# Kernel optimization log

Measured on AMD Instinct MI355X. Metric: run time of the kernel, lower is better.

The kernel has to match this reference:

```python
import jax, jax.numpy as jnp
import numpy as np

N = 50000        # nodes
E = 800000       # edges (avg degree 16)
F_IN = 128       # in_channels
HID = 32         # hidden_channels per head
H = 8            # heads
DH = HID * H     # 256, concat dim
NC = {'TL': 12, 'YL': 30, 'TS': 60, 'TZ': 120}
NEG_SLOPE = 0.2  # PyG GATConv default


def setup_inputs() -> dict:
    key = jax.random.key(0)
    ks = jax.random.split(key, 40)
    rn = lambda k, s, sc=0.1: jax.random.normal(k, s, jnp.float32) * sc
    inp = {}
    inp['x'] = jax.random.normal(ks[0], (N, F_IN), jnp.float32)
    inp['edge_index'] = jax.random.randint(ks[1], (2, E), 0, N, dtype=jnp.int64)
    # conv1: in -> H x HID (concat)
    inp['W1'] = rn(ks[2], (F_IN, DH)); inp['a1s'] = rn(ks[3], (H, HID)); inp['a1d'] = rn(ks[4], (H, HID)); inp['b1'] = jnp.zeros((DH,), jnp.float32)
    # conv2: DH -> H x HID (concat)
    inp['W2'] = rn(ks[5], (DH, DH)); inp['a2s'] = rn(ks[6], (H, HID)); inp['a2d'] = rn(ks[7], (H, HID)); inp['b2'] = jnp.zeros((DH,), jnp.float32)
    # task heads: DH -> C, heads=1, concat=False
    i = 8
    for t, c in NC.items():
        inp['W_' + t] = rn(ks[i], (DH, c)); i += 1
        inp['as_' + t] = rn(ks[i], (1, c)); i += 1
        inp['ad_' + t] = rn(ks[i], (1, c)); i += 1
        inp['b_' + t] = jnp.zeros((c,), jnp.float32)
    return inp


def gat_conv(x, src, dst, W, a_s, a_d, b, concat):
    """PyG-style GATConv (eval mode, self-loops already in src/dst)."""
    n = x.shape[0]
    heads, out_ch = a_s.shape
    h = (x @ W).reshape(n, heads, out_ch)                 # [N,H,C]
    alpha_s = jnp.einsum('nhc,hc->nh', h, a_s)            # [N,H]
    alpha_d = jnp.einsum('nhc,hc->nh', h, a_d)
    e = jax.nn.leaky_relu(alpha_s[src] + alpha_d[dst], NEG_SLOPE)   # [E,H]
    # numerically-stable segment softmax over incoming edges of each dst
    m = jax.ops.segment_max(e, dst, num_segments=n)
    ex = jnp.exp(e - m[dst])
    denom = jax.ops.segment_sum(ex, dst, num_segments=n)
    alpha = ex / (denom[dst] + 1e-16)                     # [E,H]
    out = jax.ops.segment_sum(alpha[:, :, None] * h[src], dst, num_segments=n)  # [N,H,C]
    out = out.reshape(n, heads * out_ch) if concat else out.mean(axis=1)
    return out + b


def reference(x, edge_index, W1, a1s, a1d, b1, W2, a2s, a2d, b2,
              W_TL, as_TL, ad_TL, b_TL, W_YL, as_YL, ad_YL, b_YL,
              W_TS, as_TS, ad_TS, b_TS, W_TZ, as_TZ, ad_TZ, b_TZ):
    n = x.shape[0]
    loop = jnp.arange(n, dtype=edge_index.dtype)
    src = jnp.concatenate([edge_index[0], loop])
    dst = jnp.concatenate([edge_index[1], loop])
    h = jax.nn.elu(gat_conv(x, src, dst, W1, a1s, a1d, b1, True))
    h = gat_conv(h, src, dst, W2, a2s, a2d, b2, True)
    tl = jax.nn.log_softmax(gat_conv(h, src, dst, W_TL, as_TL, ad_TL, b_TL, False), axis=1)
    yl = jax.nn.log_softmax(gat_conv(h, src, dst, W_YL, as_YL, ad_YL, b_YL, False), axis=1)
    ts = jax.nn.log_softmax(gat_conv(h, src, dst, W_TS, as_TS, ad_TS, b_TS, False), axis=1)
    tz = jax.nn.log_softmax(gat_conv(h, src, dst, W_TZ, as_TZ, ad_TZ, b_TZ, False), axis=1)
    return (tl, yl, ts, tz)
```

## Files before the change

### kernel.cpp

```cpp
#include <hip/hip_runtime.h>
#include <math.h>


#define NEG_SLOPE 0.2f

typedef short s8v __attribute__((ext_vector_type(8)));
typedef short s4v __attribute__((ext_vector_type(4)));
typedef float f4v __attribute__((ext_vector_type(4)));

__device__ __forceinline__ short f2bf(float x) {
    unsigned u = __float_as_uint(x);
    u += 0x7fffu + ((u >> 16) & 1u);
    return (short)(u >> 16);
}
__device__ __forceinline__ float bf2f(short b) {
    return __uint_as_float(((unsigned)(unsigned short)b) << 16);
}
__device__ __forceinline__ void split2(float x, short& h, short& l) {
    h = f2bf(x);
    l = f2bf(x - bf2f(h));
}
__device__ __forceinline__ float4 bf4_to_f4(s4v v) {
    return make_float4(bf2f(v[0]), bf2f(v[1]), bf2f(v[2]), bf2f(v[3]));
}


__global__ void init_kernel(int* __restrict__ deg, int* __restrict__ cursor, int n) {
    int i = blockIdx.x * blockDim.x + threadIdx.x;
    if (i < n) { deg[i] = 1; cursor[i] = 0; }
}

__global__ void count_kernel(const int* __restrict__ dst, int* __restrict__ deg, int E) {
    int i = blockIdx.x * blockDim.x + threadIdx.x;
    if (i < E) atomicAdd(&deg[dst[i]], 1);
}

__global__ __launch_bounds__(1024) void scan_kernel(const int* __restrict__ deg,
                                                    int* __restrict__ rowstart, int n) {
    __shared__ int sh[1024];
    __shared__ int carry_sh;
    if (threadIdx.x == 0) { carry_sh = 0; rowstart[0] = 0; }
    __syncthreads();
    for (int base = 0; base < n; base += 8192) {
        int vals[8];
        int sum = 0;
        int i0 = base + threadIdx.x * 8;
        #pragma unroll
        for (int j = 0; j < 8; ++j) {
            int i = i0 + j;
            int v = (i < n) ? deg[i] : 0;
            sum += v;
            vals[j] = sum;
        }
        sh[threadIdx.x] = sum;
        __syncthreads();
        for (int off = 1; off < 1024; off <<= 1) {
            int t = (threadIdx.x >= (unsigned)off) ? sh[threadIdx.x - off] : 0;
            __syncthreads();
            sh[threadIdx.x] += t;
            __syncthreads();
        }
        int excl = sh[threadIdx.x] - sum + carry_sh;
        #pragma unroll
        for (int j = 0; j < 8; ++j) {
            int i = i0 + j;
            if (i < n) rowstart[i + 1] = excl + vals[j];
        }
        __syncthreads();
        if (threadIdx.x == 0) carry_sh += sh[1023];
        __syncthreads();
    }
}

__global__ void scatter_kernel(const int* __restrict__ src, const int* __restrict__ dst,
                               const int* __restrict__ rowstart, int* __restrict__ cursor,
                               int* __restrict__ csr, int* __restrict__ csrd, int E, int n) {
    int i = blockIdx.x * blockDim.x + threadIdx.x;
    if (i >= E + n) return;
    int s, d;
    if (i < E) { s = src[i]; d = dst[i]; }
    else       { s = d = i - E; }
    int p = atomicAdd(&cursor[d], 1);
    int slot = rowstart[d] + p;
    csr[slot] = s;
    csrd[slot] = d;
}


__global__ void split_a_kernel(const float* __restrict__ A, short* __restrict__ Ah,
                               short* __restrict__ Al, int n4) {
    int i = blockIdx.x * blockDim.x + threadIdx.x;
    if (i >= n4) return;
    float4 v = ((const float4*)A)[i];
    short h0, h1, h2, h3, l0, l1, l2, l3;
    split2(v.x, h0, l0); split2(v.y, h1, l1);
    split2(v.z, h2, l2); split2(v.w, h3, l3);
    s4v hv = {h0, h1, h2, h3};
    s4v lv = {l0, l1, l2, l3};
    ((s4v*)Ah)[i] = hv;
    ((s4v*)Al)[i] = lv;
}

__global__ void split_bt_kernel(const float* __restrict__ B, short* __restrict__ Bh,
                                short* __restrict__ Bl, int K, int Nc, int kshift) {
    int idx = blockIdx.x * blockDim.x + threadIdx.x;
    if (idx >= Nc * K) return;
    int n = idx >> kshift;
    int k = idx & (K - 1);
    float v = B[(size_t)k * Nc + n];
    short h, l; split2(v, h, l);
    Bh[idx] = h;
    Bl[idx] = l;
}

__global__ void fold_alpha8_kernel(const float* __restrict__ W,
                                   const float* __restrict__ a_s, const float* __restrict__ a_d,
                                   short* __restrict__ Bth, short* __restrict__ Btl,
                                   int K, int Nfeat) {
    int idx = blockIdx.x * blockDim.x + threadIdx.x;
    if (idx >= K * 16) return;
    int j = idx / K, k = idx % K;
    int h = j & 7;
    const float* av = ((j < 8) ? a_s : a_d) + h * 32;
    const float* wp = W + (size_t)k * 256 + h * 32;
    float s = 0.f;
    #pragma unroll
    for (int c = 0; c < 32; ++c) s += wp[c] * av[c];
    short hi, lo; split2(s, hi, lo);
    size_t off = (size_t)(Nfeat + j) * K + k;
    Bth[off] = hi; Btl[off] = lo;
}

__global__ void fold_alpha4_kernel(const float* __restrict__ Wcat,
                                   const float* __restrict__ ascat, const float* __restrict__ adcat,
                                   short* __restrict__ Bth, short* __restrict__ Btl) {
    int idx = blockIdx.x * blockDim.x + threadIdx.x;
    if (idx >= 256 * 8) return;
    int j = idx >> 8, k = idx & 255;
    const int CO[4] = {0, 12, 42, 102};
    const int CL[4] = {12, 30, 60, 120};
    int t = j & 3;
    const float* av = ((j < 4) ? ascat : adcat) + CO[t];
    const float* wp = Wcat + (size_t)k * 222 + CO[t];
    float s = 0.f;
    for (int c = 0; c < CL[t]; ++c) s += wp[c] * av[c];
    short hi, lo; split2(s, hi, lo);
    size_t off = (size_t)(222 + j) * 256 + k;
    Bth[off] = hi; Btl[off] = lo;
}


#define MB 128
#define NB 64
#define KS 32

__global__ __launch_bounds__(256) void gemm_mfma_kernel(
        const short* __restrict__ Ah_g, const short* __restrict__ Al_g,
        const short* __restrict__ Bth_g, const short* __restrict__ Btl_g,
        short* __restrict__ Cb, int cb_stride,
        float* __restrict__ als, float* __restrict__ ald, int nsplit,
        int M, int K, int Nfeat, int NcExt) {
    __shared__ __align__(16) short Ah[MB][40];
    __shared__ __align__(16) short Al[MB][40];
    __shared__ __align__(16) short Bh[NB][40];
    __shared__ __align__(16) short Bl[NB][40];

    int t = threadIdx.x;
    int lane = t & 63, w = t >> 6;
    int quad = lane >> 4, l16 = lane & 15;
    int row0 = blockIdx.y * MB, col0 = blockIdx.x * NB;

    f4v acc[2][4];
    #pragma unroll
    for (int mt = 0; mt < 2; ++mt)
        #pragma unroll
        for (int nt = 0; nt < 4; ++nt)
            acc[mt][nt] = (f4v){0.f, 0.f, 0.f, 0.f};

    for (int k0 = 0; k0 < K; k0 += KS) {
        __syncthreads();
        #pragma unroll
        for (int i = 0; i < 2; ++i) {
            int u = i * 256 + t;
            int r = u >> 2, kk = (u & 3) * 8;
            int gr = row0 + r;
            s8v vh = {0, 0, 0, 0, 0, 0, 0, 0};
            s8v vl = {0, 0, 0, 0, 0, 0, 0, 0};
            if (gr < M) {
                vh = *(const s8v*)(Ah_g + (size_t)gr * K + k0 + kk);
                vl = *(const s8v*)(Al_g + (size_t)gr * K + k0 + kk);
            }
            *(s8v*)&Ah[r][kk] = vh;
            *(s8v*)&Al[r][kk] = vl;
        }
        {
            int n = t >> 2, kk = (t & 3) * 8;
            int gc = col0 + n;
            s8v vh = {0, 0, 0, 0, 0, 0, 0, 0};
            s8v vl = {0, 0, 0, 0, 0, 0, 0, 0};
            if (gc < NcExt) {
                vh = *(const s8v*)(Bth_g + (size_t)gc * K + k0 + kk);
                vl = *(const s8v*)(Btl_g + (size_t)gc * K + k0 + kk);
            }
            *(s8v*)&Bh[n][kk] = vh;
            *(s8v*)&Bl[n][kk] = vl;
        }
        __syncthreads();

        int kb = quad * 8;
        s8v a_h[2], a_l[2], b_h[4], b_l[4];
        #pragma unroll
        for (int mt = 0; mt < 2; ++mt) {
            int r = w * 32 + mt * 16 + l16;
            a_h[mt] = *(const s8v*)&Ah[r][kb];
            a_l[mt] = *(const s8v*)&Al[r][kb];
        }
        #pragma unroll
        for (int nt = 0; nt < 4; ++nt) {
            int c = nt * 16 + l16;
            b_h[nt] = *(const s8v*)&Bh[c][kb];
            b_l[nt] = *(const s8v*)&Bl[c][kb];
        }
        #pragma unroll
        for (int mt = 0; mt < 2; ++mt)
            #pragma unroll
            for (int nt = 0; nt < 4; ++nt) {
                acc[mt][nt] = __builtin_amdgcn_mfma_f32_16x16x32_bf16(
                    a_h[mt], b_h[nt], acc[mt][nt], 0, 0, 0);
                acc[mt][nt] = __builtin_amdgcn_mfma_f32_16x16x32_bf16(
                    a_h[mt], b_l[nt], acc[mt][nt], 0, 0, 0);
                acc[mt][nt] = __builtin_amdgcn_mfma_f32_16x16x32_bf16(
                    a_l[mt], b_h[nt], acc[mt][nt], 0, 0, 0);
            }
    }

    #pragma unroll
    for (int mt = 0; mt < 2; ++mt) {
        #pragma unroll
        for (int nt = 0; nt < 4; ++nt) {
            int gc = col0 + nt * 16 + l16;
            if (gc >= NcExt) continue;
            #pragma unroll
            for (int r = 0; r < 4; ++r) {
                int gr = row0 + w * 32 + mt * 16 + quad * 4 + r;
                if (gr >= M) continue;
                float v = acc[mt][nt][r];
                if (gc < Nfeat) {
                    Cb[(size_t)gr * cb_stride + gc] = f2bf(v);
                } else {
                    int j = gc - Nfeat;
                    if (j < nsplit)            als[(size_t)gr * nsplit + j] = v;
                    else if (j < 2 * nsplit)   ald[(size_t)gr * nsplit + (j - nsplit)] = v;
                }
            }
        }
    }
}


__global__ void ew8_kernel(const float* __restrict__ als, const float* __restrict__ ald,
                           const int* __restrict__ csr, const int* __restrict__ csrd,
                           float* __restrict__ ew, int M) {
    int i = blockIdx.x * blockDim.x + threadIdx.x;
    if (i >= M) return;
    int s = csr[i], d = csrd[i];
    const float4* ap = (const float4*)(als + (size_t)s * 8);
    const float4* dp = (const float4*)(ald + (size_t)d * 8);
    float4 a0 = ap[0], a1 = ap[1];
    float4 d0 = dp[0], d1 = dp[1];
    float v[8] = {a0.x + d0.x, a0.y + d0.y, a0.z + d0.z, a0.w + d0.w,
                  a1.x + d1.x, a1.y + d1.y, a1.z + d1.z, a1.w + d1.w};
    float w[8];
    #pragma unroll
    for (int h = 0; h < 8; ++h) {
        float x = v[h];
        x = (x > 0.f) ? x : NEG_SLOPE * x;
        w[h] = __expf(x);
    }
    float4* op = (float4*)(ew + (size_t)i * 8);
    op[0] = make_float4(w[0], w[1], w[2], w[3]);
    op[1] = make_float4(w[4], w[5], w[6], w[7]);
}


__global__ __launch_bounds__(256) void gat_gather_kernel(
        const short* __restrict__ hb, const float* __restrict__ ew,
        const int* __restrict__ rowstart, const int* __restrict__ csr,
        const float* __restrict__ bias, short* __restrict__ oh, short* __restrict__ ol,
        int n, int elu) {
    int wid  = blockIdx.x * 4 + (threadIdx.x >> 6);
    int lane = threadIdx.x & 63;
    if (wid >= n) return;
    int row = rowstart[wid];
    int deg = rowstart[wid + 1] - row;
    int hp = lane >> 3;
    int ch = lane * 4;
    const int* cp = csr + row;
    const float* wp = ew + (size_t)row * 8 + hp;

    float4 acc = {0.f, 0.f, 0.f, 0.f};
    float wsum = 0.f;
    int e = 0;
    for (; e + 4 <= deg; e += 4) {
        int s0 = cp[e], s1 = cp[e + 1], s2 = cp[e + 2], s3 = cp[e + 3];
        float w0 = wp[(size_t)(e + 0) * 8];
        float w1 = wp[(size_t)(e + 1) * 8];
        float w2 = wp[(size_t)(e + 2) * 8];
        float w3 = wp[(size_t)(e + 3) * 8];
        float4 h0 = bf4_to_f4(*(const s4v*)(hb + (size_t)s0 * 256 + ch));
        float4 h1 = bf4_to_f4(*(const s4v*)(hb + (size_t)s1 * 256 + ch));
        float4 h2 = bf4_to_f4(*(const s4v*)(hb + (size_t)s2 * 256 + ch));
        float4 h3 = bf4_to_f4(*(const s4v*)(hb + (size_t)s3 * 256 + ch));
        acc.x += w0 * h0.x + w1 * h1.x + w2 * h2.x + w3 * h3.x;
        acc.y += w0 * h0.y + w1 * h1.y + w2 * h2.y + w3 * h3.y;
        acc.z += w0 * h0.z + w1 * h1.z + w2 * h2.z + w3 * h3.z;
        acc.w += w0 * h0.w + w1 * h1.w + w2 * h2.w + w3 * h3.w;
        wsum += (w0 + w1) + (w2 + w3);
    }
    for (; e < deg; ++e) {
        int s0 = cp[e];
        float w0 = wp[(size_t)e * 8];
        float4 h0 = bf4_to_f4(*(const s4v*)(hb + (size_t)s0 * 256 + ch));
        acc.x += w0 * h0.x; acc.y += w0 * h0.y;
        acc.z += w0 * h0.z; acc.w += w0 * h0.w;
        wsum += w0;
    }
    float inv = 1.f / (wsum + 1e-16f);
    float4 b4 = *(const float4*)(bias + ch);
    float v[4] = {acc.x * inv + b4.x, acc.y * inv + b4.y,
                  acc.z * inv + b4.z, acc.w * inv + b4.w};
    if (elu) {
        #pragma unroll
        for (int j = 0; j < 4; ++j)
            v[j] = (v[j] > 0.f) ? v[j] : __expf(v[j]) - 1.f;
    }
    s4v hv, lv;
    #pragma unroll
    for (int j = 0; j < 4; ++j) { short hh, ll; split2(v[j], hh, ll); hv[j] = hh; lv[j] = ll; }
    *(s4v*)(oh + (size_t)wid * 256 + ch) = hv;
    *(s4v*)(ol + (size_t)wid * 256 + ch) = lv;
}


__global__ void pack_w_kernel(const float* __restrict__ wTL, const float* __restrict__ wYL,
                              const float* __restrict__ wTS, const float* __restrict__ wTZ,
                              const float* __restrict__ bTL, const float* __restrict__ bYL,
                              const float* __restrict__ bTS, const float* __restrict__ bTZ,
                              const float* __restrict__ asTL, const float* __restrict__ asYL,
                              const float* __restrict__ asTS, const float* __restrict__ asTZ,
                              const float* __restrict__ adTL, const float* __restrict__ adYL,
                              const float* __restrict__ adTS, const float* __restrict__ adTZ,
                              float* __restrict__ Wcat, float* __restrict__ bcat,
                              float* __restrict__ ascat, float* __restrict__ adcat) {
    int idx = blockIdx.x * blockDim.x + threadIdx.x;
    if (idx < 256 * 222) {
        int r = idx / 222, c = idx % 222;
        float v;
        if (c < 12)       v = wTL[r * 12 + c];
        else if (c < 42)  v = wYL[r * 30 + (c - 12)];
        else if (c < 102) v = wTS[r * 60 + (c - 42)];
        else              v = wTZ[r * 120 + (c - 102)];
        Wcat[idx] = v;
    }
    if (idx < 222) {
        bcat[idx]  = (idx < 12) ? bTL[idx] : (idx < 42) ? bYL[idx - 12]
                   : (idx < 102) ? bTS[idx - 42] : bTZ[idx - 102];
        ascat[idx] = (idx < 12) ? asTL[idx] : (idx < 42) ? asYL[idx - 12]
                   : (idx < 102) ? asTS[idx - 42] : asTZ[idx - 102];
        adcat[idx] = (idx < 12) ? adTL[idx] : (idx < 42) ? adYL[idx - 12]
                   : (idx < 102) ? adTS[idx - 42] : adTZ[idx - 102];
    }
}


__global__ void ew4_kernel(const float* __restrict__ ast, const float* __restrict__ adt,
                           const int* __restrict__ csr, const int* __restrict__ csrd,
                           float* __restrict__ ew, int M) {
    int i = blockIdx.x * blockDim.x + threadIdx.x;
    if (i >= M) return;
    int s = csr[i], d = csrd[i];
    float4 a = *(const float4*)(ast + (size_t)s * 4);
    float4 b = *(const float4*)(adt + (size_t)d * 4);
    float v[4] = {a.x + b.x, a.y + b.y, a.z + b.z, a.w + b.w};
    float w[4];
    #pragma unroll
    for (int t = 0; t < 4; ++t) {
        float x = v[t];
        x = (x > 0.f) ? x : NEG_SLOPE * x;
        w[t] = __expf(x);
    }
    *(float4*)(ew + (size_t)i * 4) = make_float4(w[0], w[1], w[2], w[3]);
}


__global__ __launch_bounds__(256) void task_gather_ls_kernel(
        const short* __restrict__ htb, const float* __restrict__ ew,
        const int* __restrict__ rowstart, const int* __restrict__ csr,
        const float* __restrict__ bcat, float* __restrict__ out, int n) {
    int wid  = blockIdx.x * 4 + (threadIdx.x >> 6);
    int lane = threadIdx.x & 63;
    if (wid >= n) return;
    int row = rowstart[wid];
    int deg = rowstart[wid + 1] - row;
    int ch0 = lane * 4;
    const int CO[4] = {0, 12, 42, 102};
    const int CL[4] = {12, 30, 60, 120};

    int tj[4]; bool valj[4];
    #pragma unroll
    for (int j = 0; j < 4; ++j) {
        int ch = ch0 + j;
        valj[j] = (ch < 222);
        tj[j] = (ch >= 102) ? 3 : (ch >= 42) ? 2 : (ch >= 12) ? 1 : 0;
    }
    int t_lo = tj[0], t_hi = tj[3];
    bool use_lo[4];
    #pragma unroll
    for (int j = 0; j < 4; ++j) use_lo[j] = (tj[j] == t_lo);

    const int* cp = csr + row;
    const float* wp = ew + (size_t)row * 4;

    float acc[4] = {0.f, 0.f, 0.f, 0.f};
    float ws_lo = 0.f, ws_hi = 0.f;
    int e = 0;
    for (; e + 4 <= deg; e += 4) {
        int s0 = cp[e], s1 = cp[e + 1], s2 = cp[e + 2], s3 = cp[e + 3];
        float wlo0 = wp[(size_t)(e + 0) * 4 + t_lo], whi0 = wp[(size_t)(e + 0) * 4 + t_hi];
        float wlo1 = wp[(size_t)(e + 1) * 4 + t_lo], whi1 = wp[(size_t)(e + 1) * 4 + t_hi];
        float wlo2 = wp[(size_t)(e + 2) * 4 + t_lo], whi2 = wp[(size_t)(e + 2) * 4 + t_hi];
        float wlo3 = wp[(size_t)(e + 3) * 4 + t_lo], whi3 = wp[(size_t)(e + 3) * 4 + t_hi];
        float4 h0 = bf4_to_f4(*(const s4v*)(htb + (size_t)s0 * 224 + ch0));
        float4 h1 = bf4_to_f4(*(const s4v*)(htb + (size_t)s1 * 224 + ch0));
        float4 h2 = bf4_to_f4(*(const s4v*)(htb + (size_t)s2 * 224 + ch0));
        float4 h3 = bf4_to_f4(*(const s4v*)(htb + (size_t)s3 * 224 + ch0));
        ws_lo += (wlo0 + wlo1) + (wlo2 + wlo3);
        ws_hi += (whi0 + whi1) + (whi2 + whi3);
        float hv0[4] = {h0.x, h0.y, h0.z, h0.w};
        float hv1[4] = {h1.x, h1.y, h1.z, h1.w};
        float hv2[4] = {h2.x, h2.y, h2.z, h2.w};
        float hv3[4] = {h3.x, h3.y, h3.z, h3.w};
        #pragma unroll
        for (int j = 0; j < 4; ++j) {
            float w0 = use_lo[j] ? wlo0 : whi0;
            float w1 = use_lo[j] ? wlo1 : whi1;
            float w2 = use_lo[j] ? wlo2 : whi2;
            float w3 = use_lo[j] ? wlo3 : whi3;
            acc[j] += w0 * hv0[j] + w1 * hv1[j] + w2 * hv2[j] + w3 * hv3[j];
        }
    }
    for (; e < deg; ++e) {
        int s = cp[e];
        float wlo = wp[(size_t)e * 4 + t_lo];
        float whi = wp[(size_t)e * 4 + t_hi];
        ws_lo += wlo; ws_hi += whi;
        float4 h0 = bf4_to_f4(*(const s4v*)(htb + (size_t)s * 224 + ch0));
        float hv[4] = {h0.x, h0.y, h0.z, h0.w};
        #pragma unroll
        for (int j = 0; j < 4; ++j) {
            float w = use_lo[j] ? wlo : whi;
            acc[j] += w * hv[j];
        }
    }
    float inv_lo = 1.f / (ws_lo + 1e-16f);
    float inv_hi = 1.f / (ws_hi + 1e-16f);

    float vout[4];
    float m4[4] = {-1e30f, -1e30f, -1e30f, -1e30f};
    #pragma unroll
    for (int j = 0; j < 4; ++j) {
        if (valj[j]) {
            float v = acc[j] * (use_lo[j] ? inv_lo : inv_hi) + bcat[ch0 + j];
            vout[j] = v;
            m4[tj[j]] = fmaxf(m4[tj[j]], v);
        } else vout[j] = 0.f;
    }
    #pragma unroll
    for (int off = 1; off < 64; off <<= 1)
        #pragma unroll
        for (int t = 0; t < 4; ++t) m4[t] = fmaxf(m4[t], __shfl_xor(m4[t], off));
    float s4a[4] = {0.f, 0.f, 0.f, 0.f};
    #pragma unroll
    for (int j = 0; j < 4; ++j)
        if (valj[j]) s4a[tj[j]] += __expf(vout[j] - m4[tj[j]]);
    #pragma unroll
    for (int off = 1; off < 64; off <<= 1)
        #pragma unroll
        for (int t = 0; t < 4; ++t) s4a[t] += __shfl_xor(s4a[t], off);
    float lse[4];
    #pragma unroll
    for (int t = 0; t < 4; ++t) lse[t] = m4[t] + __logf(s4a[t]);
    #pragma unroll
    for (int j = 0; j < 4; ++j) {
        if (!valj[j]) continue;
        int t = tj[j];
        out[(size_t)CO[t] * n + (size_t)wid * CL[t] + (ch0 + j - CO[t])] = vout[j] - lse[t];
    }
}


extern "C" void kernel_launch(void* const* d_in, const int* in_sizes, int n_in,
                              void* d_out, int out_size, void* d_ws, size_t ws_size,
                              hipStream_t stream) {
    const float* x   = (const float*)d_in[0];
    const int*   ei  = (const int*)d_in[1];
    const float* W1  = (const float*)d_in[2];
    const float* a1s = (const float*)d_in[3];
    const float* a1d = (const float*)d_in[4];
    const float* b1  = (const float*)d_in[5];
    const float* W2  = (const float*)d_in[6];
    const float* a2s = (const float*)d_in[7];
    const float* a2d = (const float*)d_in[8];
    const float* b2  = (const float*)d_in[9];
    const float* W_TL = (const float*)d_in[10]; const float* as_TL = (const float*)d_in[11];
    const float* ad_TL = (const float*)d_in[12]; const float* b_TL = (const float*)d_in[13];
    const float* W_YL = (const float*)d_in[14]; const float* as_YL = (const float*)d_in[15];
    const float* ad_YL = (const float*)d_in[16]; const float* b_YL = (const float*)d_in[17];
    const float* W_TS = (const float*)d_in[18]; const float* as_TS = (const float*)d_in[19];
    const float* ad_TS = (const float*)d_in[20]; const float* b_TS = (const float*)d_in[21];
    const float* W_TZ = (const float*)d_in[22]; const float* as_TZ = (const float*)d_in[23];
    const float* ad_TZ = (const float*)d_in[24]; const float* b_TZ = (const float*)d_in[25];

    const int N = in_sizes[0] / 128;
    const int E = in_sizes[1] / 2;
    const int* e_src = ei;
    const int* e_dst = ei + E;
    const int M = E + N;

    float* ws = (float*)d_ws;
    float* B1   = ws;
    float* B2   = B1 + (size_t)N * 256;
    float* B3   = B2 + (size_t)N * 256;
    float* as1  = B3 + (size_t)N * 256;
    float* ad1  = as1 + (size_t)N * 8;
    float* as2  = ad1 + (size_t)N * 8;
    float* ad2  = as2 + (size_t)N * 8;
    float* ast  = ad2 + (size_t)N * 8;
    float* adt  = ast + (size_t)N * 4;
    float* Wcat = adt + (size_t)N * 4;
    float* bcat = Wcat + 256 * 222;
    float* ascat = bcat + 224;
    float* adcat = ascat + 224;
    int* deg      = (int*)(adcat + 224);
    int* rowstart = deg + N;
    int* cursor   = rowstart + (N + 1);
    int* csr      = cursor + N;
    int* csrd     = csr + M;
    uintptr_t wsp = (uintptr_t)(csrd + M);
    wsp = (wsp + 15) & ~(uintptr_t)15;
    short* W1h = (short*)wsp;
    short* W1l = W1h + 272 * 128;
    short* W2h = W1l + 272 * 128;
    short* W2l = W2h + 272 * 256;
    short* Wth = W2l + 272 * 256;
    short* Wtl = Wth + 230 * 256;
    short* Xh  = (short*)B1;
    short* Xl  = Xh + (size_t)N * 128;
    short* Sh  = (short*)B1;
    short* Sl  = Sh + (size_t)N * 256;
    short* Th  = (short*)B1;
    short* Tl  = Th + (size_t)N * 256;
    short* h1b = (short*)B2;
    short* h2b = (short*)B2;
    short* htb = (short*)B2;
    float* ew1 = B3;
    float* ew2 = B3;
    float* ewt = B3;

    float* out = (float*)d_out;

    const int B = 256;
    init_kernel<<<(N + B - 1) / B, B, 0, stream>>>(deg, cursor, N);
    count_kernel<<<(E + B - 1) / B, B, 0, stream>>>(e_dst, deg, E);
    scan_kernel<<<1, 1024, 0, stream>>>(deg, rowstart, N);
    scatter_kernel<<<(M + B - 1) / B, B, 0, stream>>>(e_src, e_dst, rowstart, cursor, csr, csrd, E, N);
    pack_w_kernel<<<(256 * 222 + B - 1) / B, B, 0, stream>>>(W_TL, W_YL, W_TS, W_TZ,
        b_TL, b_YL, b_TS, b_TZ, as_TL, as_YL, as_TS, as_TZ, ad_TL, ad_YL, ad_TS, ad_TZ,
        Wcat, bcat, ascat, adcat);
    split_bt_kernel<<<(256 * 128 + B - 1) / B, B, 0, stream>>>(W1, W1h, W1l, 128, 256, 7);
    split_bt_kernel<<<(256 * 256 + B - 1) / B, B, 0, stream>>>(W2, W2h, W2l, 256, 256, 8);
    split_bt_kernel<<<(222 * 256 + B - 1) / B, B, 0, stream>>>(Wcat, Wth, Wtl, 256, 222, 8);
    fold_alpha8_kernel<<<(128 * 16 + B - 1) / B, B, 0, stream>>>(W1, a1s, a1d, W1h, W1l, 128, 256);
    fold_alpha8_kernel<<<(256 * 16 + B - 1) / B, B, 0, stream>>>(W2, a2s, a2d, W2h, W2l, 256, 256);
    fold_alpha4_kernel<<<(256 * 8 + B - 1) / B, B, 0, stream>>>(Wcat, ascat, adcat, Wth, Wtl);
    split_a_kernel<<<((N * 128 / 4) + B - 1) / B, B, 0, stream>>>(x, Xh, Xl, N * 128 / 4);
    {
        dim3 g((272 + NB - 1) / NB, (N + MB - 1) / MB);
        gemm_mfma_kernel<<<g, 256, 0, stream>>>(Xh, Xl, W1h, W1l, h1b, 256,
                                                as1, ad1, 8, N, 128, 256, 272);
    }
    ew8_kernel<<<(M + B - 1) / B, B, 0, stream>>>(as1, ad1, csr, csrd, ew1, M);
    gat_gather_kernel<<<(N + 3) / 4, 256, 0, stream>>>(h1b, ew1, rowstart, csr, b1, Sh, Sl, N, 1);
    {
        dim3 g((272 + NB - 1) / NB, (N + MB - 1) / MB);
        gemm_mfma_kernel<<<g, 256, 0, stream>>>(Sh, Sl, W2h, W2l, h2b, 256,
                                                as2, ad2, 8, N, 256, 256, 272);
    }
    ew8_kernel<<<(M + B - 1) / B, B, 0, stream>>>(as2, ad2, csr, csrd, ew2, M);
    gat_gather_kernel<<<(N + 3) / 4, 256, 0, stream>>>(h2b, ew2, rowstart, csr, b2, Th, Tl, N, 0);
    {
        dim3 g((230 + NB - 1) / NB, (N + MB - 1) / MB);
        gemm_mfma_kernel<<<g, 256, 0, stream>>>(Th, Tl, Wth, Wtl, htb, 224,
                                                ast, adt, 4, N, 256, 222, 230);
    }
    ew4_kernel<<<(M + B - 1) / B, B, 0, stream>>>(ast, adt, csr, csrd, ewt, M);
    task_gather_ls_kernel<<<(N + 3) / 4, 256, 0, stream>>>(htb, ewt, rowstart, csr, bcat, out, N);
}
```

Before: 710.4 us.

## Drop low-part bf16 split of activations and simplify task log-softmax reductions

Activations fed to the three GEMMs are now rounded to a single bf16 value, not split into hi/lo parts. This removes the lo arrays, their global writes and reads, the lo LDS tile, and one of the three MFMAs per tile. Weights keep their hi/lo split. Separately, the task-head log-softmax drops its dynamically indexed per-task arrays in favour of lo/hi selects, to avoid private-memory spills. Accuracy falls to roughly bf16 on the activation side, which risks tolerance failures.

```diff
diff --git a/kernel.cpp b/kernel.cpp
--- a/kernel.cpp
+++ b/kernel.cpp
@@ -87,18 +87,12 @@
 }
 
 
-__global__ void split_a_kernel(const float* __restrict__ A, short* __restrict__ Ah,
-                               short* __restrict__ Al, int n4) {
+__global__ void tobf_kernel(const float* __restrict__ A, short* __restrict__ Ah, int n4) {
     int i = blockIdx.x * blockDim.x + threadIdx.x;
     if (i >= n4) return;
     float4 v = ((const float4*)A)[i];
-    short h0, h1, h2, h3, l0, l1, l2, l3;
-    split2(v.x, h0, l0); split2(v.y, h1, l1);
-    split2(v.z, h2, l2); split2(v.w, h3, l3);
-    s4v hv = {h0, h1, h2, h3};
-    s4v lv = {l0, l1, l2, l3};
+    s4v hv = {f2bf(v.x), f2bf(v.y), f2bf(v.z), f2bf(v.w)};
     ((s4v*)Ah)[i] = hv;
-    ((s4v*)Al)[i] = lv;
 }
 
 __global__ void split_bt_kernel(const float* __restrict__ B, short* __restrict__ Bh,
@@ -155,13 +149,12 @@
 #define KS 32
 
 __global__ __launch_bounds__(256) void gemm_mfma_kernel(
-        const short* __restrict__ Ah_g, const short* __restrict__ Al_g,
+        const short* __restrict__ Ah_g,
         const short* __restrict__ Bth_g, const short* __restrict__ Btl_g,
         short* __restrict__ Cb, int cb_stride,
         float* __restrict__ als, float* __restrict__ ald, int nsplit,
         int M, int K, int Nfeat, int NcExt) {
     __shared__ __align__(16) short Ah[MB][40];
-    __shared__ __align__(16) short Al[MB][40];
     __shared__ __align__(16) short Bh[NB][40];
     __shared__ __align__(16) short Bl[NB][40];
 
@@ -185,13 +178,8 @@
             int r = u >> 2, kk = (u & 3) * 8;
             int gr = row0 + r;
             s8v vh = {0, 0, 0, 0, 0, 0, 0, 0};
-            s8v vl = {0, 0, 0, 0, 0, 0, 0, 0};
-            if (gr < M) {
-                vh = *(const s8v*)(Ah_g + (size_t)gr * K + k0 + kk);
-                vl = *(const s8v*)(Al_g + (size_t)gr * K + k0 + kk);
-            }
+            if (gr < M) vh = *(const s8v*)(Ah_g + (size_t)gr * K + k0 + kk);
             *(s8v*)&Ah[r][kk] = vh;
-            *(s8v*)&Al[r][kk] = vl;
         }
         {
             int n = t >> 2, kk = (t & 3) * 8;
@@ -208,12 +196,11 @@
         __syncthreads();
 
         int kb = quad * 8;
-        s8v a_h[2], a_l[2], b_h[4], b_l[4];
+        s8v a_f[2], b_h[4], b_l[4];
         #pragma unroll
         for (int mt = 0; mt < 2; ++mt) {
             int r = w * 32 + mt * 16 + l16;
-            a_h[mt] = *(const s8v*)&Ah[r][kb];
-            a_l[mt] = *(const s8v*)&Al[r][kb];
+            a_f[mt] = *(const s8v*)&Ah[r][kb];
         }
         #pragma unroll
         for (int nt = 0; nt < 4; ++nt) {
@@ -226,11 +213,9 @@
             #pragma unroll
             for (int nt = 0; nt < 4; ++nt) {
                 acc[mt][nt] = __builtin_amdgcn_mfma_f32_16x16x32_bf16(
-                    a_h[mt], b_h[nt], acc[mt][nt], 0, 0, 0);
+                    a_f[mt], b_h[nt], acc[mt][nt], 0, 0, 0);
                 acc[mt][nt] = __builtin_amdgcn_mfma_f32_16x16x32_bf16(
-                    a_h[mt], b_l[nt], acc[mt][nt], 0, 0, 0);
-                acc[mt][nt] = __builtin_amdgcn_mfma_f32_16x16x32_bf16(
-                    a_l[mt], b_h[nt], acc[mt][nt], 0, 0, 0);
+                    a_f[mt], b_l[nt], acc[mt][nt], 0, 0, 0);
             }
     }
 
@@ -286,8 +271,7 @@
 __global__ __launch_bounds__(256) void gat_gather_kernel(
         const short* __restrict__ hb, const float* __restrict__ ew,
         const int* __restrict__ rowstart, const int* __restrict__ csr,
-        const float* __restrict__ bias, short* __restrict__ oh, short* __restrict__ ol,
-        int n, int elu) {
+        const float* __restrict__ bias, short* __restrict__ oh, int n, int elu) {
     int wid  = blockIdx.x * 4 + (threadIdx.x >> 6);
     int lane = threadIdx.x & 63;
     if (wid >= n) return;
@@ -334,11 +318,8 @@
         for (int j = 0; j < 4; ++j)
             v[j] = (v[j] > 0.f) ? v[j] : __expf(v[j]) - 1.f;
     }
-    s4v hv, lv;
-    #pragma unroll
-    for (int j = 0; j < 4; ++j) { short hh, ll; split2(v[j], hh, ll); hv[j] = hh; lv[j] = ll; }
+    s4v hv = {f2bf(v[0]), f2bf(v[1]), f2bf(v[2]), f2bf(v[3])};
     *(s4v*)(oh + (size_t)wid * 256 + ch) = hv;
-    *(s4v*)(ol + (size_t)wid * 256 + ch) = lv;
 }
 
 
@@ -393,6 +374,13 @@
 }
 
 
+__device__ __forceinline__ float sel4(int t, float v0, float v1, float v2, float v3) {
+    return (t == 0) ? v0 : (t == 1) ? v1 : (t == 2) ? v2 : v3;
+}
+__device__ __forceinline__ int sel4i(int t, int v0, int v1, int v2, int v3) {
+    return (t == 0) ? v0 : (t == 1) ? v1 : (t == 2) ? v2 : v3;
+}
+
 __global__ __launch_bounds__(256) void task_gather_ls_kernel(
         const short* __restrict__ htb, const float* __restrict__ ew,
         const int* __restrict__ rowstart, const int* __restrict__ csr,
@@ -403,20 +391,22 @@
     int row = rowstart[wid];
     int deg = rowstart[wid + 1] - row;
     int ch0 = lane * 4;
-    const int CO[4] = {0, 12, 42, 102};
-    const int CL[4] = {12, 30, 60, 120};
-
-    int tj[4]; bool valj[4];
-    #pragma unroll
-    for (int j = 0; j < 4; ++j) {
-        int ch = ch0 + j;
-        valj[j] = (ch < 222);
-        tj[j] = (ch >= 102) ? 3 : (ch >= 42) ? 2 : (ch >= 12) ? 1 : 0;
-    }
-    int t_lo = tj[0], t_hi = tj[3];
-    bool use_lo[4];
-    #pragma unroll
-    for (int j = 0; j < 4; ++j) use_lo[j] = (tj[j] == t_lo);
+
+    bool valj[4]; bool lo_j[4];
+    int t_lo, t_hi;
+    {
+        int tj0 = (ch0 >= 102) ? 3 : (ch0 >= 42) ? 2 : (ch0 >= 12) ? 1 : 0;
+        int ch3 = ch0 + 3;
+        int tj3 = (ch3 >= 102) ? 3 : (ch3 >= 42) ? 2 : (ch3 >= 12) ? 1 : 0;
+        t_lo = tj0; t_hi = tj3;
+        #pragma unroll
+        for (int j = 0; j < 4; ++j) {
+            int ch = ch0 + j;
+            valj[j] = (ch < 222);
+            int tj = (ch >= 102) ? 3 : (ch >= 42) ? 2 : (ch >= 12) ? 1 : 0;
+            lo_j[j] = (tj == t_lo);
+        }
+    }
 
     const int* cp = csr + row;
     const float* wp = ew + (size_t)row * 4;
@@ -442,10 +432,10 @@
         float hv3[4] = {h3.x, h3.y, h3.z, h3.w};
         #pragma unroll
         for (int j = 0; j < 4; ++j) {
-            float w0 = use_lo[j] ? wlo0 : whi0;
-            float w1 = use_lo[j] ? wlo1 : whi1;
-            float w2 = use_lo[j] ? wlo2 : whi2;
-            float w3 = use_lo[j] ? wlo3 : whi3;
+            float w0 = lo_j[j] ? wlo0 : whi0;
+            float w1 = lo_j[j] ? wlo1 : whi1;
+            float w2 = lo_j[j] ? wlo2 : whi2;
+            float w3 = lo_j[j] ? wlo3 : whi3;
             acc[j] += w0 * hv0[j] + w1 * hv1[j] + w2 * hv2[j] + w3 * hv3[j];
         }
     }
@@ -457,44 +447,69 @@
         float4 h0 = bf4_to_f4(*(const s4v*)(htb + (size_t)s * 224 + ch0));
         float hv[4] = {h0.x, h0.y, h0.z, h0.w};
         #pragma unroll
-        for (int j = 0; j < 4; ++j) {
-            float w = use_lo[j] ? wlo : whi;
-            acc[j] += w * hv[j];
-        }
+        for (int j = 0; j < 4; ++j)
+            acc[j] += (lo_j[j] ? wlo : whi) * hv[j];
     }
     float inv_lo = 1.f / (ws_lo + 1e-16f);
     float inv_hi = 1.f / (ws_hi + 1e-16f);
 
     float vout[4];
-    float m4[4] = {-1e30f, -1e30f, -1e30f, -1e30f};
+    float m_lo = -1e30f, m_hi = -1e30f;
+    #pragma unroll
+    for (int j = 0; j < 4; ++j) {
+        float v = 0.f;
+        if (valj[j]) {
+            v = acc[j] * (lo_j[j] ? inv_lo : inv_hi) + bcat[ch0 + j];
+            if (lo_j[j]) m_lo = fmaxf(m_lo, v); else m_hi = fmaxf(m_hi, v);
+        }
+        vout[j] = v;
+    }
+    float m0 = -1e30f, m1 = -1e30f, m2 = -1e30f, m3 = -1e30f;
+    m0 = (t_lo == 0) ? fmaxf(m0, m_lo) : m0;  m0 = (t_hi == 0) ? fmaxf(m0, m_hi) : m0;
+    m1 = (t_lo == 1) ? fmaxf(m1, m_lo) : m1;  m1 = (t_hi == 1) ? fmaxf(m1, m_hi) : m1;
+    m2 = (t_lo == 2) ? fmaxf(m2, m_lo) : m2;  m2 = (t_hi == 2) ? fmaxf(m2, m_hi) : m2;
+    m3 = (t_lo == 3) ? fmaxf(m3, m_lo) : m3;  m3 = (t_hi == 3) ? fmaxf(m3, m_hi) : m3;
+    #pragma unroll
+    for (int off = 1; off < 64; off <<= 1) {
+        m0 = fmaxf(m0, __shfl_xor(m0, off));
+        m1 = fmaxf(m1, __shfl_xor(m1, off));
+        m2 = fmaxf(m2, __shfl_xor(m2, off));
+        m3 = fmaxf(m3, __shfl_xor(m3, off));
+    }
+    float mt_lo = sel4(t_lo, m0, m1, m2, m3);
+    float mt_hi = sel4(t_hi, m0, m1, m2, m3);
+    float s_lo = 0.f, s_hi = 0.f;
     #pragma unroll
     for (int j = 0; j < 4; ++j) {
         if (valj[j]) {
-            float v = acc[j] * (use_lo[j] ? inv_lo : inv_hi) + bcat[ch0 + j];
-            vout[j] = v;
-            m4[tj[j]] = fmaxf(m4[tj[j]], v);
-        } else vout[j] = 0.f;
-    }
-    #pragma unroll
-    for (int off = 1; off < 64; off <<= 1)
-        #pragma unroll
-        for (int t = 0; t < 4; ++t) m4[t] = fmaxf(m4[t], __shfl_xor(m4[t], off));
-    float s4a[4] = {0.f, 0.f, 0.f, 0.f};
-    #pragma unroll
-    for (int j = 0; j < 4; ++j)
-        if (valj[j]) s4a[tj[j]] += __expf(vout[j] - m4[tj[j]]);
-    #pragma unroll
-    for (int off = 1; off < 64; off <<= 1)
-        #pragma unroll
-        for (int t = 0; t < 4; ++t) s4a[t] += __shfl_xor(s4a[t], off);
-    float lse[4];
-    #pragma unroll
-    for (int t = 0; t < 4; ++t) lse[t] = m4[t] + __logf(s4a[t]);
+            if (lo_j[j]) s_lo += __expf(vout[j] - mt_lo);
+            else         s_hi += __expf(vout[j] - mt_hi);
+        }
+    }
+    float s0 = ((t_lo == 0) ? s_lo : 0.f) + ((t_hi == 0 && t_hi != t_lo) ? s_hi : 0.f);
+    float s1 = ((t_lo == 1) ? s_lo : 0.f) + ((t_hi == 1 && t_hi != t_lo) ? s_hi : 0.f);
+    float s2 = ((t_lo == 2) ? s_lo : 0.f) + ((t_hi == 2 && t_hi != t_lo) ? s_hi : 0.f);
+    float s3 = ((t_lo == 3) ? s_lo : 0.f) + ((t_hi == 3 && t_hi != t_lo) ? s_hi : 0.f);
+    #pragma unroll
+    for (int off = 1; off < 64; off <<= 1) {
+        s0 += __shfl_xor(s0, off);
+        s1 += __shfl_xor(s1, off);
+        s2 += __shfl_xor(s2, off);
+        s3 += __shfl_xor(s3, off);
+    }
+    float l0 = m0 + __logf(s0), l1 = m1 + __logf(s1);
+    float l2 = m2 + __logf(s2), l3 = m3 + __logf(s3);
+    float lse_lo = sel4(t_lo, l0, l1, l2, l3);
+    float lse_hi = sel4(t_hi, l0, l1, l2, l3);
+    int co_lo = sel4i(t_lo, 0, 12, 42, 102), cl_lo = sel4i(t_lo, 12, 30, 60, 120);
+    int co_hi = sel4i(t_hi, 0, 12, 42, 102), cl_hi = sel4i(t_hi, 12, 30, 60, 120);
     #pragma unroll
     for (int j = 0; j < 4; ++j) {
         if (!valj[j]) continue;
-        int t = tj[j];
-        out[(size_t)CO[t] * n + (size_t)wid * CL[t] + (ch0 + j - CO[t])] = vout[j] - lse[t];
+        int co = lo_j[j] ? co_lo : co_hi;
+        int cl = lo_j[j] ? cl_lo : cl_hi;
+        float lse = lo_j[j] ? lse_lo : lse_hi;
+        out[(size_t)co * n + (size_t)wid * cl + (ch0 + j - co)] = vout[j] - lse;
     }
 }
 
@@ -555,11 +570,8 @@
     short* Wth = W2l + 272 * 256;
     short* Wtl = Wth + 230 * 256;
     short* Xh  = (short*)B1;
-    short* Xl  = Xh + (size_t)N * 128;
     short* Sh  = (short*)B1;
-    short* Sl  = Sh + (size_t)N * 256;
     short* Th  = (short*)B1;
-    short* Tl  = Th + (size_t)N * 256;
     short* h1b = (short*)B2;
     short* h2b = (short*)B2;
     short* htb = (short*)B2;
@@ -583,24 +595,24 @@
     fold_alpha8_kernel<<<(128 * 16 + B - 1) / B, B, 0, stream>>>(W1, a1s, a1d, W1h, W1l, 128, 256);
     fold_alpha8_kernel<<<(256 * 16 + B - 1) / B, B, 0, stream>>>(W2, a2s, a2d, W2h, W2l, 256, 256);
     fold_alpha4_kernel<<<(256 * 8 + B - 1) / B, B, 0, stream>>>(Wcat, ascat, adcat, Wth, Wtl);
-    split_a_kernel<<<((N * 128 / 4) + B - 1) / B, B, 0, stream>>>(x, Xh, Xl, N * 128 / 4);
+    tobf_kernel<<<((N * 128 / 4) + B - 1) / B, B, 0, stream>>>(x, Xh, N * 128 / 4);
     {
         dim3 g((272 + NB - 1) / NB, (N + MB - 1) / MB);
-        gemm_mfma_kernel<<<g, 256, 0, stream>>>(Xh, Xl, W1h, W1l, h1b, 256,
+        gemm_mfma_kernel<<<g, 256, 0, stream>>>(Xh, W1h, W1l, h1b, 256,
                                                 as1, ad1, 8, N, 128, 256, 272);
     }
     ew8_kernel<<<(M + B - 1) / B, B, 0, stream>>>(as1, ad1, csr, csrd, ew1, M);
-    gat_gather_kernel<<<(N + 3) / 4, 256, 0, stream>>>(h1b, ew1, rowstart, csr, b1, Sh, Sl, N, 1);
+    gat_gather_kernel<<<(N + 3) / 4, 256, 0, stream>>>(h1b, ew1, rowstart, csr, b1, Sh, N, 1);
     {
         dim3 g((272 + NB - 1) / NB, (N + MB - 1) / MB);
-        gemm_mfma_kernel<<<g, 256, 0, stream>>>(Sh, Sl, W2h, W2l, h2b, 256,
+        gemm_mfma_kernel<<<g, 256, 0, stream>>>(Sh, W2h, W2l, h2b, 256,
                                                 as2, ad2, 8, N, 256, 256, 272);
     }
     ew8_kernel<<<(M + B - 1) / B, B, 0, stream>>>(as2, ad2, csr, csrd, ew2, M);
-    gat_gather_kernel<<<(N + 3) / 4, 256, 0, stream>>>(h2b, ew2, rowstart, csr, b2, Th, Tl, N, 0);
+    gat_gather_kernel<<<(N + 3) / 4, 256, 0, stream>>>(h2b, ew2, rowstart, csr, b2, Th, N, 0);
     {
         dim3 g((230 + NB - 1) / NB, (N + MB - 1) / MB);
-        gemm_mfma_kernel<<<g, 256, 0, stream>>>(Th, Tl, Wth, Wtl, htb, 224,
+        gemm_mfma_kernel<<<g, 256, 0, stream>>>(Th, Wth, Wtl, htb, 224,
                                                 ast, adt, 4, N, 256, 222, 230);
     }
     ew4_kernel<<<(M + B - 1) / B, B, 0, stream>>>(ast, adt, csr, csrd, ewt, M);
```

New measurement: 642.7 us. 9.5% less time.
